# Kernel tuning notes

Hardware: AMD Instinct MI355X
Metric: run time of the kernel (lower is better)

The kernel has to match this reference:

```python
import jax, jax.numpy as jnp
import numpy as np
import math

# ---- constants lifted verbatim from the torch source ----
PMLX = 10; PX = 400; TX = PMLX + PX + PMLX          # txsize = 420
PMLY = 10; PY = 400; TY = PMLY + PY + PMLY          # tysize = 420
CX = TX // 2; CY = TY // 2
EPS0 = 1e-9 / 36 / math.pi
MU0 = 4 * math.pi * 1e-7
C0 = 1.0 / math.sqrt(MU0 * EPS0)
DX = 2.5e-8; DY = 2.5e-8
DT = 0.99 / C0 / math.sqrt((1.0 / DX) ** 2 + (1.0 / DY) ** 2)
EPSR_INF = 5.283
EPS_INF = EPS0 * EPSR_INF
F0 = 5.47e14; BW = 0.1 * F0
T = math.sqrt(2.0) * math.sqrt(math.log(2.0)) / (math.pi * BW)
NSTEPS = 200   # reduced from 16000 for the correctness baseline; same per-step math


def setup_inputs() -> dict:
    # Lorentz (complex-pole) silver model from param(): pole/residue -> a0,a1,b0,b1,b2
    pr, pi_ = -4.8113e12, 6.8512e13
    rr, ri = 4.9581e14, -1.511e18
    a0 = -2.0 * (pr * rr + pi_ * ri)
    a1 = 2.0 * rr
    b0 = pr * pr + pi_ * pi_
    b1 = -2.0 * pr
    b2 = 1.0
    den = b0 * DT * DT + 2 * b1 * DT + 4 * b2
    Ca = np.array([-(2 * b0 * DT * DT - 8 * b2) / den], np.float32)
    Cb = np.array([-(b0 * DT * DT - 2 * b1 * DT + 4 * b2) / den], np.float32)
    Cc = np.array([(2 * a0 * EPS0 * DT + 4 * a1 * EPS0) / den], np.float32)
    Cd = np.array([-(8 * a1 * EPS0) / den], np.float32)
    Ce = np.array([(-2 * a0 * EPS0 * DT + 4 * a1 * EPS0) / den], np.float32)
    temp1 = float(Cc[0])                       # sum over tot_pol = 1 pole
    denom = EPS_INF / DT + 0.5 * temp1
    C1 = np.full((TX + 1, TY + 1), (EPS_INF / DT) / denom, np.float32)
    C2 = np.full((TX + 1, TY + 1), 0.5 / denom, np.float32)
    Cb_dx = np.full((TX + 1, TY + 1), 1.0 / denom / DX, np.float32)
    Cb_dy = np.full((TX + 1, TY + 1), 1.0 / denom / DY, np.float32)
    dbhx = np.full((TX + 1, TY), DT / MU0 / DY, np.float32)   # Hx curl coeff
    dbhy = np.full((TX, TY + 1), DT / MU0 / DX, np.float32)   # Hy curl coeff
    # polynomial-graded PML conductivity profiles (pml_param)
    m = 4
    eta0 = 120.0 * math.pi
    smax = 0.8 * (m + 1) / (eta0 * DX)

    def prof(n, npml, off):
        k = np.arange(n, dtype=np.float64)
        dl = np.clip(npml - k - off, 0.0, None) / npml   # depth into left PML
        dr = np.clip(k + off - (n - 1 - npml), 0.0, None) / npml
        return (smax * (dl ** m + dr ** m)).astype(np.float32)

    sig_ex = prof(TX + 1, PMLX, 0.0)
    sig_ey = prof(TY + 1, PMLY, 0.0)
    sig_hx = prof(TX, PMLX, 0.5)   # H nodes on half-grid
    sig_hy = prof(TY, PMLY, 0.5)
    # Gaussian-modulated sine soft source at the grid center
    t = np.arange(NSTEPS, dtype=np.float64) * DT
    src = (np.exp(-(((t - 4 * T) / T) ** 2)) * np.sin(2 * math.pi * F0 * (t - 4 * T))).astype(np.float32)
    return {
        "src": jnp.asarray(src), "C1": jnp.asarray(C1), "C2": jnp.asarray(C2),
        "Cb_dx": jnp.asarray(Cb_dx), "Cb_dy": jnp.asarray(Cb_dy),
        "dbhx": jnp.asarray(dbhx), "dbhy": jnp.asarray(dbhy),
        "Ca": jnp.asarray(Ca), "Cb": jnp.asarray(Cb), "Cc": jnp.asarray(Cc),
        "Cd": jnp.asarray(Cd), "Ce": jnp.asarray(Ce),
        "sig_ex": jnp.asarray(sig_ex), "sig_ey": jnp.asarray(sig_ey),
        "sig_hx": jnp.asarray(sig_hx), "sig_hy": jnp.asarray(sig_hy),
        "n_steps": NSTEPS,
    }


def reference(src, C1, C2, Cb_dx, Cb_dy, dbhx, dbhy, Ca, Cb, Cc, Cd, Ce,
              sig_ex, sig_ey, sig_hx, sig_hy, n_steps):
    # PML damping factors (exponential time-stepping of the conductive loss)
    de = jnp.exp(-(sig_ex[:, None] + sig_ey[None, :]) * (DT / EPS0))     # (421,421) for Ez
    dhx = jnp.exp(-(sig_ex[:, None] + sig_hy[None, :]) * (DT / MU0))     # (421,420) for Hx
    dhy = jnp.exp(-(sig_hx[:, None] + sig_ey[None, :]) * (DT / MU0))     # (420,421) for Hy
    # PEC outer boundary mask
    mask = jnp.pad(jnp.ones((TX - 1, TY - 1), de.dtype), ((1, 1), (1, 1)))
    ca = Ca[:, None, None]; cb = Cb[:, None, None]; cc = Cc[:, None, None]
    cd = Cd[:, None, None]; ce = Ce[:, None, None]

    def step(carry, s):
        Ez, Eold, Hx, Hy, Jz, Jold = carry
        # H-field Yee updates with PML damping
        Hx = dhx * (Hx - dbhx * (Ez[:, 1:] - Ez[:, :-1]))
        Hy = dhy * (Hy + dbhy * (Ez[1:, :] - Ez[:-1, :]))
        # curls onto Ez nodes (interior), zero-padded at PEC boundary
        curlHy = jnp.pad(Hy[1:, :] - Hy[:-1, :], ((1, 1), (0, 0)))       # (421,421)
        curlHx = jnp.pad(Hx[:, 1:] - Hx[:, :-1], ((0, 0), (1, 1)))       # (421,421)
        # Lorentz ADE dispersion source term (tot_pol summed; Cc*Ez^{n+1} folded into C1/C2/Cb_*)
        Phi = jnp.sum((ca + 1.0) * Jz + cb * Jold + cd * Ez[None] + ce * Eold[None], axis=0)
        Ez_new = mask * de * (C1 * Ez + Cb_dx * curlHy - Cb_dy * curlHx - C2 * Phi)
        Ez_new = Ez_new.at[CX, CY].add(s)                                 # soft point source
        # polarization current recurrence
        Jz_new = ca * Jz + cb * Jold + cc * Ez_new[None] + cd * Ez[None] + ce * Eold[None]
        return (Ez_new, Ez, Hx, Hy, Jz_new, Jz), None

    z = jnp.zeros((TX + 1, TY + 1), src.dtype)
    init = (z, z,
            jnp.zeros((TX + 1, TY), src.dtype),
            jnp.zeros((TX, TY + 1), src.dtype),
            jnp.zeros((1, TX + 1, TY + 1), src.dtype),
            jnp.zeros((1, TX + 1, TY + 1), src.dtype))
    (Ez, _, _, _, _, _), _ = jax.lax.scan(step, init, src[:n_steps])
    return Ez
```

## Files before the change

### kernel.cpp

```cpp
#include <hip/hip_runtime.h>
#include <math.h>

#define NXr 421
#define CXr 210
#define NSTEPS_C 200

#define Bt   16
#define Kt   8
#define EXT  32
#define LROWS (EXT + 2)
#define SPITCH 36
#define RING_N (2 * SPITCH + (LROWS - 2) * 4)
#define NBLK 27
#define NPHASE (NSTEPS_C / Kt)

#define PP   448
#define PAD  8
#define CP   (CXr + PAD)
#define FSZ  (PP * PP)

#define SB   (CP - 32)
#define SEED_STEPS 32
#define SROWS 66
#define SPITCH2 68
#define RING_N2 (2 * SPITCH2 + (SROWS - 2) * 4)

typedef float v2f __attribute__((ext_vector_type(2)));
static __device__ __forceinline__ v2f mk2(float x, float y)
{ v2f r; r.x = x; r.y = y; return r; }

struct PParams {
    float *aEz, *aJz, *aU, *aHx, *aHy;
    float *bEz, *bJz, *bU, *bHx, *bHy;
    const float *dexP, *deyP, *aexP, *aeyP, *ahxP, *ahyP;
    const float *C1a, *C2a, *Cbdxa, *Cbdya;
    const float *Caa, *Cba, *Cca, *Cda, *Cea, *dbhxa, *dbhya;
    const float *src;
};

__global__ void init_kernel(const float* __restrict__ sig_ex,
                            const float* __restrict__ sig_ey,
                            const float* __restrict__ sig_hx,
                            const float* __restrict__ sig_hy,
                            float de_fac, float dh_fac,
                            float* __restrict__ zero_base, int n_zero,
                            float* __restrict__ dexP, float* __restrict__ deyP,
                            float* __restrict__ aexP, float* __restrict__ aeyP,
                            float* __restrict__ ahxP, float* __restrict__ ahyP)
{
    int t = blockIdx.x * blockDim.x + threadIdx.x;
    int stride = gridDim.x * blockDim.x;
    for (int k = t; k < n_zero; k += stride) zero_base[k] = 0.0f;
    if (t < PP) {
        int g = t - PAD;
        dexP[t] = (g >= 1 && g <= NXr - 2) ? expf(-sig_ex[g] * de_fac) : 0.0f;
        deyP[t] = (g >= 1 && g <= NXr - 2) ? expf(-sig_ey[g] * de_fac) : 0.0f;
        aexP[t] = (g >= 0 && g <  NXr)     ? expf(-sig_ex[g] * dh_fac) : 0.0f;
        aeyP[t] = (g >= 0 && g <  NXr)     ? expf(-sig_ey[g] * dh_fac) : 0.0f;
        ahxP[t] = (g >= 0 && g <  NXr - 1) ? expf(-sig_hx[g] * dh_fac) : 0.0f;
        ahyP[t] = (g >= 0 && g <  NXr - 1) ? expf(-sig_hy[g] * dh_fac) : 0.0f;
    }
}

__global__ __launch_bounds__(1024)
void seed_kernel(PParams p)
{
    __shared__ __align__(16) float sE[2][SROWS][SPITCH2];

    const int tid = threadIdx.x;
    const int tj = tid & 31, ti = tid >> 5;
    const int li0 = 2 * ti, lj0 = 2 * tj;
    const int r0 = SB + li0, c0 = SB + lj0;

    const float ca = p.Caa[0], cb = p.Cba[0], cc = p.Cca[0];
    const float cd = p.Cda[0], ce = p.Cea[0];
    const float ca1f = ca + 1.0f;
    const float C1f = p.C1a[0], C2f = p.C2a[0];
    const float cbdxf = p.Cbdxa[0], cbdyf = p.Cbdya[0];
    const float dbhx0 = p.dbhxa[0], dbhy0 = p.dbhya[0];

    const v2f vca1 = mk2(ca1f, ca1f), vcb = mk2(cb, cb), vcc = mk2(cc, cc);
    const v2f vcd = mk2(cd, cd), vce = mk2(ce, ce);
    const v2f vC1 = mk2(C1f, C1f), vC2 = mk2(C2f, C2f);
    const v2f vbx = mk2(cbdxf, cbdxf), vby = mk2(cbdyf, cbdyf);
    const v2f vhx = mk2(dbhx0, dbhx0), vhy = mk2(dbhy0, dbhy0);

    v2f dHx[2], dHy[2], dE[2], dHyU, srcw[2];
    float dHxL[2];
#pragma unroll
    for (int a = 0; a < 2; ++a) {
        float aex = p.aexP[r0 + a], ahxv = p.ahxP[r0 + a], dex = p.dexP[r0 + a];
        dHx[a] = mk2(aex * p.ahyP[c0], aex * p.ahyP[c0 + 1]);
        dHy[a] = mk2(ahxv * p.aeyP[c0], ahxv * p.aeyP[c0 + 1]);
        dE[a]  = mk2(dex * p.deyP[c0], dex * p.deyP[c0 + 1]);
        srcw[a] = mk2(((r0 + a == CP) && (c0 == CP)) ? 1.0f : 0.0f,
                      ((r0 + a == CP) && (c0 + 1 == CP)) ? 1.0f : 0.0f);
    }
    {
        float ahxU = p.ahxP[r0 - 1];
        float ahyL = p.ahyP[c0 - 1];
        dHyU = mk2(ahxU * p.aeyP[c0], ahxU * p.aeyP[c0 + 1]);
        dHxL[0] = p.aexP[r0] * ahyL;
        dHxL[1] = p.aexP[r0 + 1] * ahyL;
    }

    v2f ez[2] = {}, jz[2] = {}, uu[2] = {}, hx[2] = {}, hy[2] = {};
    v2f hyU = {};
    float hxL[2] = {};

    for (int z = tid; z < 2 * RING_N2; z += 1024) {
        int b = (z >= RING_N2) ? 1 : 0;
        int r = b ? z - RING_N2 : z;
        int row, col;
        if (r < 2 * SPITCH2) { row = (r < SPITCH2) ? 0 : (SROWS - 1); col = r % SPITCH2; }
        else { int rr = r - 2 * SPITCH2; row = 1 + (rr >> 2); int c = rr & 3;
               col = (c < 2) ? c : c + 64; }
        sE[b][row][col] = 0.0f;
    }

    float svl[SEED_STEPS];
#pragma unroll
    for (int s = 0; s < SEED_STEPS; ++s) svl[s] = p.src[s];

    for (int s = 0; s < SEED_STEPS; ++s) {
        float (*S)[SPITCH2] = sE[s & 1];
        *(float2*)&S[1 + li0][2 + lj0] = make_float2(ez[0].x, ez[0].y);
        *(float2*)&S[2 + li0][2 + lj0] = make_float2(ez[1].x, ez[1].y);

        hy[0] = dHy[0] * (hy[0] + vhy * (ez[1] - ez[0]));
        v2f w0 = hx[0] + vhx * ez[0];
        v2f w1 = hx[1] + vhx * ez[1];

        v2f phi0 = vca1 * jz[0] + vcd * ez[0] + uu[0];
        v2f phi1 = vca1 * jz[1] + vcd * ez[1] + uu[1];
        v2f base0 = vC1 * ez[0] - vC2 * phi0;
        v2f base1 = vC1 * ez[1] - vC2 * phi1;
        v2f pj0 = phi0 - jz[0];
        v2f pj1 = phi1 - jz[1];
        uu[0] = vcb * jz[0] + vce * ez[0];
        uu[1] = vcb * jz[1] + vce * ez[1];

        __syncthreads();

        float eR0 = S[1 + li0][4 + lj0];
        float eR1 = S[2 + li0][4 + lj0];
        float2 eDf = *(float2*)&S[3 + li0][2 + lj0];
        float2 eUf = *(float2*)&S[li0][2 + lj0];
        float eL0 = S[1 + li0][1 + lj0];
        float eL1 = S[2 + li0][1 + lj0];
        v2f eD = mk2(eDf.x, eDf.y), eU = mk2(eUf.x, eUf.y);

        v2f sh0 = mk2(ez[0].y, eR0);
        v2f sh1 = mk2(ez[1].y, eR1);
        hx[0] = dHx[0] * (w0 - vhx * sh0);
        hx[1] = dHx[1] * (w1 - vhx * sh1);
        hy[1] = dHy[1] * (hy[1] + vhy * (eD - ez[1]));

        hyU = dHyU * (hyU + vhy * (ez[0] - eU));
        hxL[0] = dHxL[0] * (hxL[0] - dbhx0 * (ez[0].x - eL0));
        hxL[1] = dHxL[1] * (hxL[1] - dbhx0 * (ez[1].x - eL1));

        v2f cHy0 = hy[0] - hyU;
        v2f cHy1 = hy[1] - hy[0];
        v2f cHx0 = hx[0] - mk2(hxL[0], hx[0].x);
        v2f cHx1 = hx[1] - mk2(hxL[1], hx[1].x);

        float sv = svl[s];
        v2f vsv = mk2(sv, sv);
        v2f en0 = dE[0] * (base0 + vbx * cHy0 - vby * cHx0) + srcw[0] * vsv;
        v2f en1 = dE[1] * (base1 + vbx * cHy1 - vby * cHx1) + srcw[1] * vsv;
        jz[0] = pj0 + vcc * en0;
        jz[1] = pj1 + vcc * en1;
        ez[0] = en0;
        ez[1] = en1;
    }

#pragma unroll
    for (int a = 0; a < 2; ++a) {
        int g = (r0 + a) * PP + c0;
        *(float2*)&p.aEz[g] = make_float2(ez[a].x, ez[a].y);
        *(float2*)&p.aJz[g] = make_float2(jz[a].x, jz[a].y);
        *(float2*)&p.aU[g]  = make_float2(uu[a].x, uu[a].y);
        *(float2*)&p.aHx[g] = make_float2(hx[a].x, hx[a].y);
        *(float2*)&p.aHy[g] = make_float2(hy[a].x, hy[a].y);
    }
}

__global__ __launch_bounds__(256)
void phase_kernel(PParams p, int t, int b0, float* __restrict__ out,
                  int writeOut)
{
    __shared__ __align__(16) float sEz[2][LROWS][SPITCH];

    const int tid = threadIdx.x;
    const int tj = tid & 15, ti = tid >> 4;
    const int li0 = 2 * ti, lj0 = 2 * tj;

    const int gx = (int)gridDim.x;
    int orig = (int)blockIdx.y * gx + (int)blockIdx.x;
    int nwg = gx * gx;
    int q = nwg >> 3, rr = nwg & 7;
    int xcd = orig & 7, kk = orig >> 3;
    int nid = (xcd < rr ? xcd * (q + 1) : rr * (q + 1) + (xcd - rr) * q) + kk;
    int bx = nid % gx, by = nid / gx;

    const int r0 = (bx + b0) * Bt + li0;
    const int c0 = (by + b0) * Bt + lj0;

    const float ca = p.Caa[0], cb = p.Cba[0], cc = p.Cca[0];
    const float cd = p.Cda[0], ce = p.Cea[0];
    const float ca1f = ca + 1.0f;
    const float C1f = p.C1a[0], C2f = p.C2a[0];
    const float cbdxf = p.Cbdxa[0], cbdyf = p.Cbdya[0];
    const float dbhx0 = p.dbhxa[0], dbhy0 = p.dbhya[0];

    const v2f vca1 = mk2(ca1f, ca1f), vcb = mk2(cb, cb), vcc = mk2(cc, cc);
    const v2f vcd = mk2(cd, cd), vce = mk2(ce, ce);
    const v2f vC1 = mk2(C1f, C1f), vC2 = mk2(C2f, C2f);
    const v2f vbx = mk2(cbdxf, cbdxf), vby = mk2(cbdyf, cbdyf);
    const v2f vhx = mk2(dbhx0, dbhx0), vhy = mk2(dbhy0, dbhy0);

    v2f dHx[2], dHy[2], dE[2], dHyU, srcw[2];
    float dHxL[2];
#pragma unroll
    for (int a = 0; a < 2; ++a) {
        float aex = p.aexP[r0 + a], ahxv = p.ahxP[r0 + a], dex = p.dexP[r0 + a];
        dHx[a] = mk2(aex * p.ahyP[c0], aex * p.ahyP[c0 + 1]);
        dHy[a] = mk2(ahxv * p.aeyP[c0], ahxv * p.aeyP[c0 + 1]);
        dE[a]  = mk2(dex * p.deyP[c0], dex * p.deyP[c0 + 1]);
        srcw[a] = mk2(((r0 + a == CP) && (c0 == CP)) ? 1.0f : 0.0f,
                      ((r0 + a == CP) && (c0 + 1 == CP)) ? 1.0f : 0.0f);
    }
    {
        float ahxU = (r0 > 0) ? p.ahxP[r0 - 1] : 0.0f;
        float ahyL = (c0 > 0) ? p.ahyP[c0 - 1] : 0.0f;
        dHyU = mk2(ahxU * p.aeyP[c0], ahxU * p.aeyP[c0 + 1]);
        dHxL[0] = p.aexP[r0] * ahyL;
        dHxL[1] = p.aexP[r0 + 1] * ahyL;
    }

    const bool odd = (t & 1) != 0;
    const float* cEz = odd ? p.bEz : p.aEz;
    const float* cJz = odd ? p.bJz : p.aJz;
    const float* cU  = odd ? p.bU  : p.aU;
    const float* cHx = odd ? p.bHx : p.aHx;
    const float* cHy = odd ? p.bHy : p.aHy;
    float* nEz = odd ? p.aEz : p.bEz;
    float* nJz = odd ? p.aJz : p.bJz;
    float* nU  = odd ? p.aU  : p.bU;
    float* nHx = odd ? p.aHx : p.bHx;
    float* nHy = odd ? p.aHy : p.bHy;

    for (int z = tid; z < 2 * RING_N; z += 256) {
        int b = (z >= RING_N) ? 1 : 0;
        int r = b ? z - RING_N : z;
        int row, col;
        if (r < 2 * SPITCH) { row = (r < SPITCH) ? 0 : (LROWS - 1); col = r % SPITCH; }
        else { int rr2 = r - 2 * SPITCH; row = 1 + (rr2 >> 2); int c = rr2 & 3;
               col = (c < 2) ? c : c + EXT; }
        sEz[b][row][col] = 0.0f;
    }

    v2f ez[2], jz[2], uu[2], hx[2], hy[2];
#pragma unroll
    for (int a = 0; a < 2; ++a) {
        int g = (r0 + a) * PP + c0;
        float2 v;
        v = *(const float2*)&cEz[g]; ez[a] = mk2(v.x, v.y);
        v = *(const float2*)&cJz[g]; jz[a] = mk2(v.x, v.y);
        v = *(const float2*)&cU[g];  uu[a] = mk2(v.x, v.y);
        v = *(const float2*)&cHx[g]; hx[a] = mk2(v.x, v.y);
        v = *(const float2*)&cHy[g]; hy[a] = mk2(v.x, v.y);
    }
    v2f hyU;
    float hxL[2];
    {
        float2 v = *(const float2*)&cHy[(r0 - 1) * PP + c0];
        hyU = mk2(v.x, v.y);
        hxL[0] = cHx[r0 * PP + c0 - 1];
        hxL[1] = cHx[(r0 + 1) * PP + c0 - 1];
    }

    const int n0 = t * Kt;
    float svl[Kt];
#pragma unroll
    for (int s = 0; s < Kt; ++s) svl[s] = p.src[n0 + s];

    for (int s = 0; s < Kt; ++s) {
        float (*S)[SPITCH] = sEz[s & 1];
        *(float2*)&S[1 + li0][2 + lj0] = make_float2(ez[0].x, ez[0].y);
        *(float2*)&S[2 + li0][2 + lj0] = make_float2(ez[1].x, ez[1].y);

        hy[0] = dHy[0] * (hy[0] + vhy * (ez[1] - ez[0]));
        v2f w0 = hx[0] + vhx * ez[0];
        v2f w1 = hx[1] + vhx * ez[1];

        v2f phi0 = vca1 * jz[0] + vcd * ez[0] + uu[0];
        v2f phi1 = vca1 * jz[1] + vcd * ez[1] + uu[1];
        v2f base0 = vC1 * ez[0] - vC2 * phi0;
        v2f base1 = vC1 * ez[1] - vC2 * phi1;
        v2f pj0 = phi0 - jz[0];
        v2f pj1 = phi1 - jz[1];
        uu[0] = vcb * jz[0] + vce * ez[0];
        uu[1] = vcb * jz[1] + vce * ez[1];

        __syncthreads();

        float eR0 = S[1 + li0][4 + lj0];
        float eR1 = S[2 + li0][4 + lj0];
        float2 eDf = *(float2*)&S[3 + li0][2 + lj0];
        float2 eUf = *(float2*)&S[li0][2 + lj0];
        float eL0 = S[1 + li0][1 + lj0];
        float eL1 = S[2 + li0][1 + lj0];
        v2f eD = mk2(eDf.x, eDf.y), eU = mk2(eUf.x, eUf.y);

        v2f sh0 = mk2(ez[0].y, eR0);
        v2f sh1 = mk2(ez[1].y, eR1);
        hx[0] = dHx[0] * (w0 - vhx * sh0);
        hx[1] = dHx[1] * (w1 - vhx * sh1);
        hy[1] = dHy[1] * (hy[1] + vhy * (eD - ez[1]));

        hyU = dHyU * (hyU + vhy * (ez[0] - eU));
        hxL[0] = dHxL[0] * (hxL[0] - dbhx0 * (ez[0].x - eL0));
        hxL[1] = dHxL[1] * (hxL[1] - dbhx0 * (ez[1].x - eL1));

        v2f cHy0 = hy[0] - hyU;
        v2f cHy1 = hy[1] - hy[0];
        v2f cHx0 = hx[0] - mk2(hxL[0], hx[0].x);
        v2f cHx1 = hx[1] - mk2(hxL[1], hx[1].x);

        float sv = svl[s];
        v2f vsv = mk2(sv, sv);
        v2f en0 = dE[0] * (base0 + vbx * cHy0 - vby * cHx0) + srcw[0] * vsv;
        v2f en1 = dE[1] * (base1 + vbx * cHy1 - vby * cHx1) + srcw[1] * vsv;
        jz[0] = pj0 + vcc * en0;
        jz[1] = pj1 + vcc * en1;
        ez[0] = en0;
        ez[1] = en1;
    }

    if (ti >= 4 && ti < 12 && tj >= 4 && tj < 12) {
#pragma unroll
        for (int a = 0; a < 2; ++a) {
            int g = (r0 + a) * PP + c0;
            *(float2*)&nEz[g] = make_float2(ez[a].x, ez[a].y);
            *(float2*)&nJz[g] = make_float2(jz[a].x, jz[a].y);
            *(float2*)&nU[g]  = make_float2(uu[a].x, uu[a].y);
            *(float2*)&nHx[g] = make_float2(hx[a].x, hx[a].y);
            *(float2*)&nHy[g] = make_float2(hy[a].x, hy[a].y);
        }
        if (writeOut) {
#pragma unroll
            for (int a = 0; a < 2; ++a) {
                int gi = r0 + a - PAD;
                if (gi < NXr) {
                    int gj = c0 - PAD;
                    if (gj < NXr)     out[gi * NXr + gj]     = ez[a].x;
                    if (gj + 1 < NXr) out[gi * NXr + gj + 1] = ez[a].y;
                }
            }
        }
    }
}

extern "C" void kernel_launch(void* const* d_in, const int* in_sizes, int n_in,
                              void* d_out, int out_size, void* d_ws, size_t ws_size,
                              hipStream_t stream)
{
    const float* src    = (const float*)d_in[0];
    const float* C1     = (const float*)d_in[1];
    const float* C2     = (const float*)d_in[2];
    const float* Cb_dx  = (const float*)d_in[3];
    const float* Cb_dy  = (const float*)d_in[4];
    const float* dbhx   = (const float*)d_in[5];
    const float* dbhy   = (const float*)d_in[6];
    const float* Ca     = (const float*)d_in[7];
    const float* Cb     = (const float*)d_in[8];
    const float* Cc     = (const float*)d_in[9];
    const float* Cd     = (const float*)d_in[10];
    const float* Ce     = (const float*)d_in[11];
    const float* sig_ex = (const float*)d_in[12];
    const float* sig_ey = (const float*)d_in[13];
    const float* sig_hx = (const float*)d_in[14];
    const float* sig_hy = (const float*)d_in[15];

    const double EPS0 = 1e-9 / 36.0 / M_PI;
    const double MU0  = 4.0 * M_PI * 1e-7;
    const double C0   = 1.0 / sqrt(MU0 * EPS0);
    const double DXd  = 2.5e-8, DYd = 2.5e-8;
    const double DT   = 0.99 / C0 / sqrt(1.0 / (DXd * DXd) + 1.0 / (DYd * DYd));
    const float de_fac = (float)(DT / EPS0);
    const float dh_fac = (float)(DT / MU0);

    float* base = (float*)d_ws;
    float* fields = base + PP;
    float* w = fields + 10 * (size_t)FSZ;
    float* dexP = w; w += PP;
    float* deyP = w; w += PP;
    float* aexP = w; w += PP;
    float* aeyP = w; w += PP;
    float* ahxP = w; w += PP;
    float* ahyP = w; w += PP;

    PParams p;
    p.aEz = fields + 0 * (size_t)FSZ;  p.aJz = fields + 1 * (size_t)FSZ;
    p.aU  = fields + 2 * (size_t)FSZ;  p.aHx = fields + 3 * (size_t)FSZ;
    p.aHy = fields + 4 * (size_t)FSZ;
    p.bEz = fields + 5 * (size_t)FSZ;  p.bJz = fields + 6 * (size_t)FSZ;
    p.bU  = fields + 7 * (size_t)FSZ;  p.bHx = fields + 8 * (size_t)FSZ;
    p.bHy = fields + 9 * (size_t)FSZ;
    p.dexP = dexP; p.deyP = deyP; p.aexP = aexP; p.aeyP = aeyP;
    p.ahxP = ahxP; p.ahyP = ahyP;
    p.C1a = C1; p.C2a = C2; p.Cbdxa = Cb_dx; p.Cbdya = Cb_dy;
    p.Caa = Ca; p.Cba = Cb; p.Cca = Cc; p.Cda = Cd; p.Cea = Ce;
    p.dbhxa = dbhx; p.dbhya = dbhy;
    p.src = src;

    init_kernel<<<512, 256, 0, stream>>>(sig_ex, sig_ey, sig_hx, sig_hy,
                                         de_fac, dh_fac,
                                         base, PP + 10 * FSZ,
                                         dexP, deyP, aexP, aeyP, ahxP, ahyP);

    seed_kernel<<<1, 1024, 0, stream>>>(p);

    dim3 blk(256);
    for (int t = 4; t < NPHASE; ++t) {
        int R  = 8 * t + 11;
        int lo = CP - R, hi = CP + R;
        int b0 = (lo - (EXT - 1)) / 16; if (b0 < 0) b0 = 0;
        int b1 = hi / 16;               if (b1 > NBLK - 1) b1 = NBLK - 1;
        dim3 g(b1 - b0 + 1, b1 - b0 + 1);
        phase_kernel<<<g, blk, 0, stream>>>(p, t, b0, (float*)d_out,
                                            (t == NPHASE - 1) ? 1 : 0);
    }
}
```

Baseline: 245.1 us.

## Merge early phases into 16-step temporally blocked kernel with larger halo tiles

Replaces the first eight 8-step phase launches (steps 32–95) with four launches of a new merged kernel that advances 16 time steps per launch, using 24x24 thread tiles with a 48-wide halo and only writing the central 16x16 region. This halves the number of launches and global round-trips during the early, small-wavefront phases. In exchange it adds more redundant halo compute, since only 64 of 576 threads write results, and uses larger shared memory and blocks. The ping-pong buffer parity is now passed explicitly to keep the remaining phase kernels consistent.

```diff
diff --git a/kernel.cpp b/kernel.cpp
--- a/kernel.cpp
+++ b/kernel.cpp
@@ -13,6 +13,13 @@
 #define RING_N (2 * SPITCH + (LROWS - 2) * 4)
 #define NBLK 27
 #define NPHASE (NSTEPS_C / Kt)
+
+#define TDIM2 24
+#define NTHR2 (TDIM2 * TDIM2)
+#define EXT2 48
+#define MROWS (EXT2 + 2)
+#define MPITCH 52
+#define MRING (2 * MPITCH + (MROWS - 2) * 4)
 
 #define PP   448
 #define PAD  8
@@ -186,14 +193,13 @@
     }
 }
 
-__global__ __launch_bounds__(256)
-void phase_kernel(PParams p, int t, int b0, float* __restrict__ out,
-                  int writeOut)
+__global__ __launch_bounds__(NTHR2)
+void merged_kernel(PParams p, int n0, int b0, int rw)
 {
-    __shared__ __align__(16) float sEz[2][LROWS][SPITCH];
+    __shared__ __align__(16) float sEz[2][MROWS][MPITCH];
 
     const int tid = threadIdx.x;
-    const int tj = tid & 15, ti = tid >> 4;
+    const int ti = tid / TDIM2, tj = tid - ti * TDIM2;
     const int li0 = 2 * ti, lj0 = 2 * tj;
 
     const int gx = (int)gridDim.x;
@@ -239,17 +245,180 @@
         dHxL[1] = p.aexP[r0 + 1] * ahyL;
     }
 
-    const bool odd = (t & 1) != 0;
-    const float* cEz = odd ? p.bEz : p.aEz;
-    const float* cJz = odd ? p.bJz : p.aJz;
-    const float* cU  = odd ? p.bU  : p.aU;
-    const float* cHx = odd ? p.bHx : p.aHx;
-    const float* cHy = odd ? p.bHy : p.aHy;
-    float* nEz = odd ? p.aEz : p.bEz;
-    float* nJz = odd ? p.aJz : p.bJz;
-    float* nU  = odd ? p.aU  : p.bU;
-    float* nHx = odd ? p.aHx : p.bHx;
-    float* nHy = odd ? p.aHy : p.bHy;
+    const float* cEz = rw ? p.bEz : p.aEz;
+    const float* cJz = rw ? p.bJz : p.aJz;
+    const float* cU  = rw ? p.bU  : p.aU;
+    const float* cHx = rw ? p.bHx : p.aHx;
+    const float* cHy = rw ? p.bHy : p.aHy;
+    float* nEz = rw ? p.aEz : p.bEz;
+    float* nJz = rw ? p.aJz : p.bJz;
+    float* nU  = rw ? p.aU  : p.bU;
+    float* nHx = rw ? p.aHx : p.bHx;
+    float* nHy = rw ? p.aHy : p.bHy;
+
+    for (int z = tid; z < 2 * MRING; z += NTHR2) {
+        int b = (z >= MRING) ? 1 : 0;
+        int r = b ? z - MRING : z;
+        int row, col;
+        if (r < 2 * MPITCH) { row = (r < MPITCH) ? 0 : (MROWS - 1); col = r % MPITCH; }
+        else { int rr2 = r - 2 * MPITCH; row = 1 + (rr2 >> 2); int c = rr2 & 3;
+               col = (c < 2) ? c : c + EXT2; }
+        sEz[b][row][col] = 0.0f;
+    }
+
+    v2f ez[2], jz[2], uu[2], hx[2], hy[2];
+#pragma unroll
+    for (int a = 0; a < 2; ++a) {
+        int g = (r0 + a) * PP + c0;
+        float2 v;
+        v = *(const float2*)&cEz[g]; ez[a] = mk2(v.x, v.y);
+        v = *(const float2*)&cJz[g]; jz[a] = mk2(v.x, v.y);
+        v = *(const float2*)&cU[g];  uu[a] = mk2(v.x, v.y);
+        v = *(const float2*)&cHx[g]; hx[a] = mk2(v.x, v.y);
+        v = *(const float2*)&cHy[g]; hy[a] = mk2(v.x, v.y);
+    }
+    v2f hyU;
+    float hxL[2];
+    {
+        float2 v = *(const float2*)&cHy[(r0 - 1) * PP + c0];
+        hyU = mk2(v.x, v.y);
+        hxL[0] = cHx[r0 * PP + c0 - 1];
+        hxL[1] = cHx[(r0 + 1) * PP + c0 - 1];
+    }
+
+    float svl[16];
+#pragma unroll
+    for (int s = 0; s < 16; ++s) svl[s] = p.src[n0 + s];
+
+    for (int s = 0; s < 16; ++s) {
+        float (*S)[MPITCH] = sEz[s & 1];
+        *(float2*)&S[1 + li0][2 + lj0] = make_float2(ez[0].x, ez[0].y);
+        *(float2*)&S[2 + li0][2 + lj0] = make_float2(ez[1].x, ez[1].y);
+
+        hy[0] = dHy[0] * (hy[0] + vhy * (ez[1] - ez[0]));
+        v2f w0 = hx[0] + vhx * ez[0];
+        v2f w1 = hx[1] + vhx * ez[1];
+
+        v2f phi0 = vca1 * jz[0] + vcd * ez[0] + uu[0];
+        v2f phi1 = vca1 * jz[1] + vcd * ez[1] + uu[1];
+        v2f base0 = vC1 * ez[0] - vC2 * phi0;
+        v2f base1 = vC1 * ez[1] - vC2 * phi1;
+        v2f pj0 = phi0 - jz[0];
+        v2f pj1 = phi1 - jz[1];
+        uu[0] = vcb * jz[0] + vce * ez[0];
+        uu[1] = vcb * jz[1] + vce * ez[1];
+
+        __syncthreads();
+
+        float eR0 = S[1 + li0][4 + lj0];
+        float eR1 = S[2 + li0][4 + lj0];
+        float2 eDf = *(float2*)&S[3 + li0][2 + lj0];
+        float2 eUf = *(float2*)&S[li0][2 + lj0];
+        float eL0 = S[1 + li0][1 + lj0];
+        float eL1 = S[2 + li0][1 + lj0];
+        v2f eD = mk2(eDf.x, eDf.y), eU = mk2(eUf.x, eUf.y);
+
+        v2f sh0 = mk2(ez[0].y, eR0);
+        v2f sh1 = mk2(ez[1].y, eR1);
+        hx[0] = dHx[0] * (w0 - vhx * sh0);
+        hx[1] = dHx[1] * (w1 - vhx * sh1);
+        hy[1] = dHy[1] * (hy[1] + vhy * (eD - ez[1]));
+
+        hyU = dHyU * (hyU + vhy * (ez[0] - eU));
+        hxL[0] = dHxL[0] * (hxL[0] - dbhx0 * (ez[0].x - eL0));
+        hxL[1] = dHxL[1] * (hxL[1] - dbhx0 * (ez[1].x - eL1));
+
+        v2f cHy0 = hy[0] - hyU;
+        v2f cHy1 = hy[1] - hy[0];
+        v2f cHx0 = hx[0] - mk2(hxL[0], hx[0].x);
+        v2f cHx1 = hx[1] - mk2(hxL[1], hx[1].x);
+
+        float sv = svl[s];
+        v2f vsv = mk2(sv, sv);
+        v2f en0 = dE[0] * (base0 + vbx * cHy0 - vby * cHx0) + srcw[0] * vsv;
+        v2f en1 = dE[1] * (base1 + vbx * cHy1 - vby * cHx1) + srcw[1] * vsv;
+        jz[0] = pj0 + vcc * en0;
+        jz[1] = pj1 + vcc * en1;
+        ez[0] = en0;
+        ez[1] = en1;
+    }
+
+    if (ti >= 8 && ti < 16 && tj >= 8 && tj < 16) {
+#pragma unroll
+        for (int a = 0; a < 2; ++a) {
+            int g = (r0 + a) * PP + c0;
+            *(float2*)&nEz[g] = make_float2(ez[a].x, ez[a].y);
+            *(float2*)&nJz[g] = make_float2(jz[a].x, jz[a].y);
+            *(float2*)&nU[g]  = make_float2(uu[a].x, uu[a].y);
+            *(float2*)&nHx[g] = make_float2(hx[a].x, hx[a].y);
+            *(float2*)&nHy[g] = make_float2(hy[a].x, hy[a].y);
+        }
+    }
+}
+
+__global__ __launch_bounds__(256)
+void phase_kernel(PParams p, int t, int b0, float* __restrict__ out,
+                  int writeOut, int rw)
+{
+    __shared__ __align__(16) float sEz[2][LROWS][SPITCH];
+
+    const int tid = threadIdx.x;
+    const int tj = tid & 15, ti = tid >> 4;
+    const int li0 = 2 * ti, lj0 = 2 * tj;
+
+    const int gx = (int)gridDim.x;
+    int orig = (int)blockIdx.y * gx + (int)blockIdx.x;
+    int nwg = gx * gx;
+    int q = nwg >> 3, rr = nwg & 7;
+    int xcd = orig & 7, kk = orig >> 3;
+    int nid = (xcd < rr ? xcd * (q + 1) : rr * (q + 1) + (xcd - rr) * q) + kk;
+    int bx = nid % gx, by = nid / gx;
+
+    const int r0 = (bx + b0) * Bt + li0;
+    const int c0 = (by + b0) * Bt + lj0;
+
+    const float ca = p.Caa[0], cb = p.Cba[0], cc = p.Cca[0];
+    const float cd = p.Cda[0], ce = p.Cea[0];
+    const float ca1f = ca + 1.0f;
+    const float C1f = p.C1a[0], C2f = p.C2a[0];
+    const float cbdxf = p.Cbdxa[0], cbdyf = p.Cbdya[0];
+    const float dbhx0 = p.dbhxa[0], dbhy0 = p.dbhya[0];
+
+    const v2f vca1 = mk2(ca1f, ca1f), vcb = mk2(cb, cb), vcc = mk2(cc, cc);
+    const v2f vcd = mk2(cd, cd), vce = mk2(ce, ce);
+    const v2f vC1 = mk2(C1f, C1f), vC2 = mk2(C2f, C2f);
+    const v2f vbx = mk2(cbdxf, cbdxf), vby = mk2(cbdyf, cbdyf);
+    const v2f vhx = mk2(dbhx0, dbhx0), vhy = mk2(dbhy0, dbhy0);
+
+    v2f dHx[2], dHy[2], dE[2], dHyU, srcw[2];
+    float dHxL[2];
+#pragma unroll
+    for (int a = 0; a < 2; ++a) {
+        float aex = p.aexP[r0 + a], ahxv = p.ahxP[r0 + a], dex = p.dexP[r0 + a];
+        dHx[a] = mk2(aex * p.ahyP[c0], aex * p.ahyP[c0 + 1]);
+        dHy[a] = mk2(ahxv * p.aeyP[c0], ahxv * p.aeyP[c0 + 1]);
+        dE[a]  = mk2(dex * p.deyP[c0], dex * p.deyP[c0 + 1]);
+        srcw[a] = mk2(((r0 + a == CP) && (c0 == CP)) ? 1.0f : 0.0f,
+                      ((r0 + a == CP) && (c0 + 1 == CP)) ? 1.0f : 0.0f);
+    }
+    {
+        float ahxU = (r0 > 0) ? p.ahxP[r0 - 1] : 0.0f;
+        float ahyL = (c0 > 0) ? p.ahyP[c0 - 1] : 0.0f;
+        dHyU = mk2(ahxU * p.aeyP[c0], ahxU * p.aeyP[c0 + 1]);
+        dHxL[0] = p.aexP[r0] * ahyL;
+        dHxL[1] = p.aexP[r0 + 1] * ahyL;
+    }
+
+    const float* cEz = rw ? p.bEz : p.aEz;
+    const float* cJz = rw ? p.bJz : p.aJz;
+    const float* cU  = rw ? p.bU  : p.aU;
+    const float* cHx = rw ? p.bHx : p.aHx;
+    const float* cHy = rw ? p.bHy : p.aHy;
+    float* nEz = rw ? p.aEz : p.bEz;
+    float* nJz = rw ? p.aJz : p.bJz;
+    float* nU  = rw ? p.aU  : p.bU;
+    float* nHx = rw ? p.aHx : p.bHx;
+    float* nHy = rw ? p.aHy : p.bHy;
 
     for (int z = tid; z < 2 * RING_N; z += 256) {
         int b = (z >= RING_N) ? 1 : 0;
@@ -423,14 +592,25 @@
 
     seed_kernel<<<1, 1024, 0, stream>>>(p);
 
+    for (int j = 0; j < 4; ++j) {
+        int R  = 16 * j + 51;
+        int lo = CP - R, hi = CP + R;
+        int b0 = (lo - (EXT2 - 1)) / Bt; if (b0 < 0) b0 = 0;
+        int b1 = hi / Bt;                if (b1 > NBLK - 1) b1 = NBLK - 1;
+        dim3 g(b1 - b0 + 1, b1 - b0 + 1);
+        merged_kernel<<<g, dim3(NTHR2), 0, stream>>>(p, 32 + 16 * j, b0,
+                                                     j & 1);
+    }
+
     dim3 blk(256);
-    for (int t = 4; t < NPHASE; ++t) {
+    for (int t = 12; t < NPHASE; ++t) {
         int R  = 8 * t + 11;
         int lo = CP - R, hi = CP + R;
         int b0 = (lo - (EXT - 1)) / 16; if (b0 < 0) b0 = 0;
         int b1 = hi / 16;               if (b1 > NBLK - 1) b1 = NBLK - 1;
         dim3 g(b1 - b0 + 1, b1 - b0 + 1);
         phase_kernel<<<g, blk, 0, stream>>>(p, t, b0, (float*)d_out,
-                                            (t == NPHASE - 1) ? 1 : 0);
+                                            (t == NPHASE - 1) ? 1 : 0,
+                                            (t - 12) & 1);
     }
 }
```

Result: no change. 245.9 us (+0.3%).
